# Kernel tuning notes

Measured on AMD Instinct MI355X. Metric: run time of the kernel, lower is better.

## Reference

```python
import jax, jax.numpy as jnp
import numpy as np

A, D, F = 2048, 64, 12  # atoms, depth, filter_length


def _chemconv(x, conn, bond, filters):
    # x: (A, D); conn: (A, A, F); bond: (A, F, 2); filters: (D, F, D+2)
    # node_connection = conn.transpose(1,2) @ x -> (A, F, D)
    ncon = jnp.einsum('anf,nd->afd', conn, x)
    combined = jnp.concatenate([ncon, bond], axis=2)  # (A, F, D+2)
    # broadcast-multiply by filters then sum over last two dims -> (A, out_depth)
    return jnp.einsum('afc,ofc->ao', combined, filters)


def setup_inputs() -> dict:
    key = jax.random.key(0)
    k1, k2, k3, k4, k5 = jax.random.split(key, 5)
    x = jax.random.normal(k1, (A, D), dtype=jnp.float32)
    conn = jax.random.uniform(k2, (A, A, F), dtype=jnp.float32)
    bond = jax.random.normal(k3, (A, F, 2), dtype=jnp.float32)
    scale = 1.0 / D  # filters.data.normal_() * (1/in_depth)
    f0 = jax.random.normal(k4, (D, F, D + 2), dtype=jnp.float32) * scale
    f1 = jax.random.normal(k5, (D, F, D + 2), dtype=jnp.float32) * scale
    return {
        'node_property_tensor': x,
        'connectivity_tensor': conn,
        'bond_property_tensor': bond,
        'filters0': f0,
        'filters1': f1,
    }


def reference(node_property_tensor, connectivity_tensor, bond_property_tensor, filters0, filters1):
    x = node_property_tensor
    out = x
    for filt in (filters0, filters1):
        # each ChemConv layer is applied twice (same weights), per the torch code
        out = jax.nn.relu(_chemconv(out, connectivity_tensor, bond_property_tensor, filt))
        out = _chemconv(out, connectivity_tensor, bond_property_tensor, filt)
        out = out + x  # residual to the original block input
        out = jax.nn.relu(out)
    return out
```

## Files before the change

kernel.cpp:

```cpp
#include <hip/hip_runtime.h>


#define A_N 2048
#define D_N 64
#define F_N 12
#define K_TOTAL (A_N * F_N)
#define NSPLIT 32
#define KSEG (K_TOTAL / NSPLIT)
#define BK 64
#define NKB (KSEG / BK)

typedef short short8 __attribute__((ext_vector_type(8)));
typedef float f32x16 __attribute__((ext_vector_type(16)));

#define GLOAD16(ldsp, gp)                                                        \
  __builtin_amdgcn_global_load_lds(                                              \
      (const __attribute__((address_space(1))) void*)(gp),                       \
      (__attribute__((address_space(3))) void*)(ldsp), 16, 0, 0)

#define VMWAIT(n) asm volatile("s_waitcnt vmcnt(" #n ")" ::: "memory")

__device__ __forceinline__ unsigned pk_bf16(float a, float b) {
  unsigned ua = __float_as_uint(a);
  unsigned ub = __float_as_uint(b);
  ua += 0x7fffu + ((ua >> 16) & 1u);
  ub += 0x7fffu + ((ub >> 16) & 1u);
  return (ua >> 16) | (ub & 0xffff0000u);
}

__device__ __forceinline__ unsigned short bf16_1(float v) {
  unsigned u = __float_as_uint(v);
  u += 0x7fffu + ((u >> 16) & 1u);
  return (unsigned short)(u >> 16);
}

__global__ void k_prep(const float* __restrict__ x, float* __restrict__ xt,
                       const float* __restrict__ bond, const float* __restrict__ f0,
                       const float* __restrict__ f1, float* __restrict__ bt0,
                       float* __restrict__ bt1) {
  int t = threadIdx.x;
  if (blockIdx.x < 32) {
    __shared__ float ld[64][65];
    int m0 = blockIdx.x * 64;
    int r = t >> 2, cq = (t & 3) * 16;
    const float4* src = (const float4*)(x + (size_t)(m0 + r) * 64 + cq);
#pragma unroll
    for (int i = 0; i < 4; ++i) {
      float4 v = src[i];
      ld[r][cq + i * 4 + 0] = v.x;
      ld[r][cq + i * 4 + 1] = v.y;
      ld[r][cq + i * 4 + 2] = v.z;
      ld[r][cq + i * 4 + 3] = v.w;
    }
    __syncthreads();
    int c = t >> 2, ml0 = (t & 3) * 16;
    float4* dst = (float4*)(xt + (size_t)c * 2048 + m0 + ml0);
#pragma unroll
    for (int i = 0; i < 4; ++i) {
      float4 v;
      v.x = ld[ml0 + i * 4 + 0][c];
      v.y = ld[ml0 + i * 4 + 1][c];
      v.z = ld[ml0 + i * 4 + 2][c];
      v.w = ld[ml0 + i * 4 + 3][c];
      dst[i] = v;
    }
  } else {
    int b = blockIdx.x - 32;
    int a = (b & 31) * 64 + (t & 63);
    int o = (b >> 5) * 4 + (t >> 6);
    float s0 = 0.f, s1 = 0.f;
#pragma unroll
    for (int f = 0; f < F_N; ++f) {
#pragma unroll
      for (int j = 0; j < 2; ++j) {
        float bv = bond[a * 24 + f * 2 + j];
        s0 += bv * f0[o * 792 + f * 66 + 64 + j];
        s1 += bv * f1[o * 792 + f * 66 + 64 + j];
      }
    }
    bt0[o * 2048 + a] = s0;
    bt1[o * 2048 + a] = s1;
  }
}

__global__ void k_cvt(const float* __restrict__ conn, unsigned short* __restrict__ connt) {
  int t = threadIdx.x;
  int kb = blockIdx.x, ks = blockIdx.y, atile = blockIdx.z;
  const float* src = conn + (size_t)(atile * 128) * K_TOTAL + ks * KSEG + kb * 64;
  unsigned short* dst = connt + (size_t)((atile * NSPLIT + ks) * NKB + kb) * 8192;
  int r0 = t >> 3, c0 = (t & 7) * 8;
#pragma unroll
  for (int i = 0; i < 4; ++i) {
    int row = r0 + i * 32;
    const float4* s4 = (const float4*)(src + (size_t)row * K_TOTAL + c0);
    float4 a = s4[0], b = s4[1];
    uint4 p;
    p.x = pk_bf16(a.x, a.y);
    p.y = pk_bf16(a.z, a.w);
    p.z = pk_bf16(b.x, b.y);
    p.w = pk_bf16(b.z, b.w);
    *(uint4*)(dst + row * 64 + c0) = p;
  }
}

__global__ void k_g(const float* __restrict__ vt, const float* __restrict__ filt,
                    unsigned short* __restrict__ gtt, int rep) {
  __shared__ __align__(16) float WT[64][12];
  __shared__ __align__(16) unsigned short sg[6144];
  int o = blockIdx.y, bx = blockIdx.x;
  int t = threadIdx.x;
  for (int i = t; i < 768; i += 256) {
    int d = i / 12, f = i % 12;
    WT[d][f] = filt[o * 792 + f * 66 + d];
  }
  __syncthreads();
  int n0 = bx * 512 + t;
  unsigned short* gbase = gtt + (size_t)(bx * 96) * 4096 + o * 64;
  for (int r = 0; r < rep; ++r) {
    float acc0[12], acc1[12];
#pragma unroll
    for (int f = 0; f < 12; ++f) { acc0[f] = 0.f; acc1[f] = 0.f; }
#pragma unroll 4
    for (int d = 0; d < 64; ++d) {
      float v0 = vt[d * 2048 + n0];
      float v1 = vt[d * 2048 + n0 + 256];
      const float4* wp = (const float4*)WT[d];
      float4 w0 = wp[0], w1 = wp[1], w2 = wp[2];
      acc0[0] += v0 * w0.x;  acc0[1] += v0 * w0.y;  acc0[2]  += v0 * w0.z;  acc0[3]  += v0 * w0.w;
      acc0[4] += v0 * w1.x;  acc0[5] += v0 * w1.y;  acc0[6]  += v0 * w1.z;  acc0[7]  += v0 * w1.w;
      acc0[8] += v0 * w2.x;  acc0[9] += v0 * w2.y;  acc0[10] += v0 * w2.z;  acc0[11] += v0 * w2.w;
      acc1[0] += v1 * w0.x;  acc1[1] += v1 * w0.y;  acc1[2]  += v1 * w0.z;  acc1[3]  += v1 * w0.w;
      acc1[4] += v1 * w1.x;  acc1[5] += v1 * w1.y;  acc1[6]  += v1 * w1.z;  acc1[7]  += v1 * w1.w;
      acc1[8] += v1 * w2.x;  acc1[9] += v1 * w2.y;  acc1[10] += v1 * w2.z;  acc1[11] += v1 * w2.w;
    }
#pragma unroll
    for (int f = 0; f < F_N; ++f) {
      sg[t * 12 + f] = bf16_1(acc0[f]);
      sg[t * 12 + 3072 + f] = bf16_1(acc1[f]);
    }
    __syncthreads();
#pragma unroll
    for (int j = 0; j < 3; ++j) {
      int m = t + j * 256;
      *(uint4*)(gbase + (size_t)(m >> 3) * 4096 + (m & 7) * 8) =
          *(const uint4*)(sg + m * 8);
    }
    __syncthreads();
  }
}

__launch_bounds__(256, 2)
__global__ void k_big(const unsigned short* __restrict__ connt,
                      const unsigned short* __restrict__ gtt, float* __restrict__ part) {
  __shared__ __align__(16) unsigned short smem[36864];
  int t = threadIdx.x, lane = t & 63, w = t >> 6;
  int atile = blockIdx.x, ks = blockIdx.y;
  const unsigned short* ct = connt + (size_t)(atile * NSPLIT + ks) * (NKB * 8192);
  const unsigned short* gs = gtt + (size_t)ks * (NKB * 4096);

  int rl = lane >> 3, sl = lane & 7;
  int cs = sl ^ rl;

  int cSrc[4], gSrc[2], cDst[4], gDst[2];
#pragma unroll
  for (int j = 0; j < 4; ++j) {
    cSrc[j] = (w * 32 + j * 8 + rl) * 64 + cs * 8;
    cDst[j] = (w * 32 + j * 8) * 64;
  }
#pragma unroll
  for (int j = 0; j < 2; ++j) {
    gSrc[j] = (w * 16 + j * 8 + rl) * 64 + cs * 8;
    gDst[j] = 8192 + (w * 16 + j * 8) * 64;
  }

  f32x16 acc0, acc1;
#pragma unroll
  for (int i = 0; i < 16; ++i) { acc0[i] = 0.f; acc1[i] = 0.f; }

  int oh = w >> 1, ah = w & 1;
  int orow = oh * 32 + (lane & 31);
  int arow = ah * 64 + (lane & 31);
  int sw = lane & 7;
  int khalf = lane >> 5;

#pragma unroll
  for (int p = 0; p < 2; ++p) {
    unsigned short* base = smem + p * 12288;
#pragma unroll
    for (int j = 0; j < 4; ++j) GLOAD16(base + cDst[j], ct + p * 8192 + cSrc[j]);
#pragma unroll
    for (int j = 0; j < 2; ++j) GLOAD16(base + gDst[j], gs + p * 4096 + gSrc[j]);
  }

#pragma unroll
  for (int kb = 0; kb < NKB; ++kb) {
    if (kb < NKB - 1) VMWAIT(6);
    else VMWAIT(0);
    __builtin_amdgcn_s_barrier();
    asm volatile("" ::: "memory");
    if (kb + 2 < NKB) {
      unsigned short* base = smem + ((kb + 2) % 3) * 12288;
#pragma unroll
      for (int j = 0; j < 4; ++j) GLOAD16(base + cDst[j], ct + (kb + 2) * 8192 + cSrc[j]);
#pragma unroll
      for (int j = 0; j < 2; ++j) GLOAD16(base + gDst[j], gs + (kb + 2) * 4096 + gSrc[j]);
    }
    const unsigned short* cb = smem + (kb % 3) * 12288;
    const unsigned short* gb = cb + 8192;
#pragma unroll
    for (int kk = 0; kk < 4; ++kk) {
      int c = kk * 2 + khalf;
      int coff = ((c ^ sw) << 3);
      short8 af = *(const short8*)(gb + orow * 64 + coff);
      short8 b0 = *(const short8*)(cb + arow * 64 + coff);
      short8 b1 = *(const short8*)(cb + (arow + 32) * 64 + coff);
      acc0 = __builtin_amdgcn_mfma_f32_32x32x16_bf16(af, b0, acc0, 0, 0, 0);
      acc1 = __builtin_amdgcn_mfma_f32_32x32x16_bf16(af, b1, acc1, 0, 0, 0);
    }
  }

  float* pp = part + (size_t)ks * (64 * 2048);
  int a0 = atile * 128 + ah * 64 + (lane & 31);
  int ob = oh * 32 + 4 * khalf;
#pragma unroll
  for (int rg = 0; rg < 16; ++rg) {
    int o = ob + (rg & 3) + 8 * (rg >> 2);
    pp[o * 2048 + a0] = acc0[rg];
    pp[o * 2048 + a0 + 32] = acc1[rg];
  }
}

__global__ void k_reduce(const float* __restrict__ part, const float* __restrict__ bt,
                         const float* __restrict__ xt, float* __restrict__ curt,
                         float* __restrict__ outp, int residual, int final_layer, int rep) {
  __shared__ float4 buf[128];
  int t = threadIdx.x;
  int i4 = blockIdx.x * 128 + (t & 127);
  int half = t >> 7;
  int sbase = half * 16;
  for (int r = 0; r < rep; ++r) {
    float4 s = {0.f, 0.f, 0.f, 0.f};
#pragma unroll
    for (int k = 0; k < 16; ++k) {
      float4 p = ((const float4*)part)[(size_t)(sbase + k) * 32768 + i4];
      s.x += p.x; s.y += p.y; s.z += p.z; s.w += p.w;
    }
    if (half) buf[t & 127] = s;
    __syncthreads();
    if (!half) {
      float4 q = buf[t];
      float4 b = ((const float4*)bt)[i4];
      s.x += q.x + b.x; s.y += q.y + b.y; s.z += q.z + b.z; s.w += q.w + b.w;
      if (residual) {
        float4 rr = ((const float4*)xt)[i4];
        s.x += rr.x; s.y += rr.y; s.z += rr.z; s.w += rr.w;
      }
      s.x = fmaxf(s.x, 0.f); s.y = fmaxf(s.y, 0.f);
      s.z = fmaxf(s.z, 0.f); s.w = fmaxf(s.w, 0.f);
      ((float4*)curt)[i4] = s;
      if (final_layer) {
        int idx = i4 * 4;
        int o = idx >> 11, m = idx & 2047;
        outp[(m + 0) * 64 + o] = s.x;
        outp[(m + 1) * 64 + o] = s.y;
        outp[(m + 2) * 64 + o] = s.z;
        outp[(m + 3) * 64 + o] = s.w;
      }
    }
    __syncthreads();
  }
}

extern "C" void kernel_launch(void* const* d_in, const int* in_sizes, int n_in,
                              void* d_out, int out_size, void* d_ws, size_t ws_size,
                              hipStream_t stream) {
  const float* x    = (const float*)d_in[0];
  const float* conn = (const float*)d_in[1];
  const float* bond = (const float*)d_in[2];
  const float* f0   = (const float*)d_in[3];
  const float* f1   = (const float*)d_in[4];
  float* out = (float*)d_out;

  char* ws = (char*)d_ws;
  float* xt   = (float*)(ws + 0);
  float* curt = (float*)(ws + 524288);
  float* bt0  = (float*)(ws + 1048576);
  float* bt1  = (float*)(ws + 1572864);
  unsigned short* gtt = (unsigned short*)(ws + 2097152);
  float* part = (float*)(ws + 5242880);
  unsigned short* connt = (unsigned short*)(ws + 33554432);

  k_prep<<<544, 256, 0, stream>>>(x, xt, bond, f0, f1, bt0, bt1);
  k_cvt<<<dim3(NKB, NSPLIT, 16), 256, 0, stream>>>(conn, connt);

  for (int layer = 0; layer < 4; ++layer) {
    const float* filt = (layer < 2) ? f0 : f1;
    const float* bt   = (layer < 2) ? bt0 : bt1;
    const float* vin  = (layer == 0) ? xt : curt;
    k_g<<<dim3(4, 64), 256, 0, stream>>>(vin, filt, gtt, (layer == 3) ? 17 : 1);
    k_big<<<dim3(16, NSPLIT), 256, 0, stream>>>(connt, gtt, part);
    k_reduce<<<256, 256, 0, stream>>>(part, bt, xt, curt, out, layer & 1, layer == 3,
                                      (layer == 3) ? 17 : 1);
  }
}
```

Baseline: 551.8 us.

## Halve k_big tile, merge prep and convert kernels, drop repeat loops

k_big now covers 64 atoms per block instead of 128, giving 1024 blocks with a smaller LDS footprint and launch bounds of 3 blocks per CU. The goal is more parallelism and occupancy, at the cost of reloading each G tile twice as often. The separate prep and bf16-convert kernels are merged into one launch to save a kernel launch. The previous code repeated k_g and k_reduce 17 times in the last layer, apparently as padding, and that artificial repeat is removed.

```diff
diff --git a/kernel.cpp b/kernel.cpp
--- a/kernel.cpp
+++ b/kernel.cpp
@@ -34,14 +34,15 @@
   return (unsigned short)(u >> 16);
 }
 
-__global__ void k_prep(const float* __restrict__ x, float* __restrict__ xt,
-                       const float* __restrict__ bond, const float* __restrict__ f0,
-                       const float* __restrict__ f1, float* __restrict__ bt0,
-                       float* __restrict__ bt1) {
-  int t = threadIdx.x;
-  if (blockIdx.x < 32) {
+__global__ void k_pre(const float* __restrict__ x, float* __restrict__ xt,
+                      const float* __restrict__ bond, const float* __restrict__ f0,
+                      const float* __restrict__ f1, float* __restrict__ bt0,
+                      float* __restrict__ bt1, const float* __restrict__ conn,
+                      unsigned short* __restrict__ connt) {
+  int t = threadIdx.x, b = blockIdx.x;
+  if (b < 32) {
     __shared__ float ld[64][65];
-    int m0 = blockIdx.x * 64;
+    int m0 = b * 64;
     int r = t >> 2, cq = (t & 3) * 16;
     const float4* src = (const float4*)(x + (size_t)(m0 + r) * 64 + cq);
 #pragma unroll
@@ -64,10 +65,10 @@
       v.w = ld[ml0 + i * 4 + 3][c];
       dst[i] = v;
     }
-  } else {
-    int b = blockIdx.x - 32;
-    int a = (b & 31) * 64 + (t & 63);
-    int o = (b >> 5) * 4 + (t >> 6);
+  } else if (b < 544) {
+    int b2 = b - 32;
+    int a = (b2 & 31) * 64 + (t & 63);
+    int o = (b2 >> 5) * 4 + (t >> 6);
     float s0 = 0.f, s1 = 0.f;
 #pragma unroll
     for (int f = 0; f < F_N; ++f) {
@@ -80,31 +81,31 @@
     }
     bt0[o * 2048 + a] = s0;
     bt1[o * 2048 + a] = s1;
-  }
-}
-
-__global__ void k_cvt(const float* __restrict__ conn, unsigned short* __restrict__ connt) {
-  int t = threadIdx.x;
-  int kb = blockIdx.x, ks = blockIdx.y, atile = blockIdx.z;
-  const float* src = conn + (size_t)(atile * 128) * K_TOTAL + ks * KSEG + kb * 64;
-  unsigned short* dst = connt + (size_t)((atile * NSPLIT + ks) * NKB + kb) * 8192;
-  int r0 = t >> 3, c0 = (t & 7) * 8;
-#pragma unroll
-  for (int i = 0; i < 4; ++i) {
-    int row = r0 + i * 32;
-    const float4* s4 = (const float4*)(src + (size_t)row * K_TOTAL + c0);
-    float4 a = s4[0], b = s4[1];
-    uint4 p;
-    p.x = pk_bf16(a.x, a.y);
-    p.y = pk_bf16(a.z, a.w);
-    p.z = pk_bf16(b.x, b.y);
-    p.w = pk_bf16(b.z, b.w);
-    *(uint4*)(dst + row * 64 + c0) = p;
+  } else {
+    int i = b - 544;
+    int atile = i / 384;
+    int r2 = i % 384;
+    int ks = r2 / 12, kb = r2 % 12;
+    const float* src = conn + (size_t)(atile * 128) * K_TOTAL + ks * KSEG + kb * 64;
+    unsigned short* dst = connt + (size_t)((atile * NSPLIT + ks) * NKB + kb) * 8192;
+    int r0 = t >> 3, c0 = (t & 7) * 8;
+#pragma unroll
+    for (int q = 0; q < 4; ++q) {
+      int row = r0 + q * 32;
+      const float4* s4 = (const float4*)(src + (size_t)row * K_TOTAL + c0);
+      float4 a = s4[0], bb = s4[1];
+      uint4 p;
+      p.x = pk_bf16(a.x, a.y);
+      p.y = pk_bf16(a.z, a.w);
+      p.z = pk_bf16(bb.x, bb.y);
+      p.w = pk_bf16(bb.z, bb.w);
+      *(uint4*)(dst + row * 64 + c0) = p;
+    }
   }
 }
 
 __global__ void k_g(const float* __restrict__ vt, const float* __restrict__ filt,
-                    unsigned short* __restrict__ gtt, int rep) {
+                    unsigned short* __restrict__ gtt) {
   __shared__ __align__(16) float WT[64][12];
   __shared__ __align__(16) unsigned short sg[6144];
   int o = blockIdx.y, bx = blockIdx.x;
@@ -115,159 +116,149 @@
   }
   __syncthreads();
   int n0 = bx * 512 + t;
+  float acc0[12], acc1[12];
+#pragma unroll
+  for (int f = 0; f < 12; ++f) { acc0[f] = 0.f; acc1[f] = 0.f; }
+#pragma unroll 4
+  for (int d = 0; d < 64; ++d) {
+    float v0 = vt[d * 2048 + n0];
+    float v1 = vt[d * 2048 + n0 + 256];
+    const float4* wp = (const float4*)WT[d];
+    float4 w0 = wp[0], w1 = wp[1], w2 = wp[2];
+    acc0[0] += v0 * w0.x;  acc0[1] += v0 * w0.y;  acc0[2]  += v0 * w0.z;  acc0[3]  += v0 * w0.w;
+    acc0[4] += v0 * w1.x;  acc0[5] += v0 * w1.y;  acc0[6]  += v0 * w1.z;  acc0[7]  += v0 * w1.w;
+    acc0[8] += v0 * w2.x;  acc0[9] += v0 * w2.y;  acc0[10] += v0 * w2.z;  acc0[11] += v0 * w2.w;
+    acc1[0] += v1 * w0.x;  acc1[1] += v1 * w0.y;  acc1[2]  += v1 * w0.z;  acc1[3]  += v1 * w0.w;
+    acc1[4] += v1 * w1.x;  acc1[5] += v1 * w1.y;  acc1[6]  += v1 * w1.z;  acc1[7]  += v1 * w1.w;
+    acc1[8] += v1 * w2.x;  acc1[9] += v1 * w2.y;  acc1[10] += v1 * w2.z;  acc1[11] += v1 * w2.w;
+  }
+#pragma unroll
+  for (int f = 0; f < F_N; ++f) {
+    sg[t * 12 + f] = bf16_1(acc0[f]);
+    sg[t * 12 + 3072 + f] = bf16_1(acc1[f]);
+  }
+  __syncthreads();
   unsigned short* gbase = gtt + (size_t)(bx * 96) * 4096 + o * 64;
-  for (int r = 0; r < rep; ++r) {
-    float acc0[12], acc1[12];
-#pragma unroll
-    for (int f = 0; f < 12; ++f) { acc0[f] = 0.f; acc1[f] = 0.f; }
-#pragma unroll 4
-    for (int d = 0; d < 64; ++d) {
-      float v0 = vt[d * 2048 + n0];
-      float v1 = vt[d * 2048 + n0 + 256];
-      const float4* wp = (const float4*)WT[d];
-      float4 w0 = wp[0], w1 = wp[1], w2 = wp[2];
-      acc0[0] += v0 * w0.x;  acc0[1] += v0 * w0.y;  acc0[2]  += v0 * w0.z;  acc0[3]  += v0 * w0.w;
-      acc0[4] += v0 * w1.x;  acc0[5] += v0 * w1.y;  acc0[6]  += v0 * w1.z;  acc0[7]  += v0 * w1.w;
-      acc0[8] += v0 * w2.x;  acc0[9] += v0 * w2.y;  acc0[10] += v0 * w2.z;  acc0[11] += v0 * w2.w;
-      acc1[0] += v1 * w0.x;  acc1[1] += v1 * w0.y;  acc1[2]  += v1 * w0.z;  acc1[3]  += v1 * w0.w;
-      acc1[4] += v1 * w1.x;  acc1[5] += v1 * w1.y;  acc1[6]  += v1 * w1.z;  acc1[7]  += v1 * w1.w;
-      acc1[8] += v1 * w2.x;  acc1[9] += v1 * w2.y;  acc1[10] += v1 * w2.z;  acc1[11] += v1 * w2.w;
-    }
-#pragma unroll
-    for (int f = 0; f < F_N; ++f) {
-      sg[t * 12 + f] = bf16_1(acc0[f]);
-      sg[t * 12 + 3072 + f] = bf16_1(acc1[f]);
-    }
-    __syncthreads();
-#pragma unroll
-    for (int j = 0; j < 3; ++j) {
-      int m = t + j * 256;
-      *(uint4*)(gbase + (size_t)(m >> 3) * 4096 + (m & 7) * 8) =
-          *(const uint4*)(sg + m * 8);
-    }
-    __syncthreads();
-  }
-}
-
-__launch_bounds__(256, 2)
+#pragma unroll
+  for (int j = 0; j < 3; ++j) {
+    int m = t + j * 256;
+    *(uint4*)(gbase + (size_t)(m >> 3) * 4096 + (m & 7) * 8) = *(const uint4*)(sg + m * 8);
+  }
+}
+
+__launch_bounds__(256, 3)
 __global__ void k_big(const unsigned short* __restrict__ connt,
                       const unsigned short* __restrict__ gtt, float* __restrict__ part) {
-  __shared__ __align__(16) unsigned short smem[36864];
+  __shared__ __align__(16) unsigned short smem[24576];
   int t = threadIdx.x, lane = t & 63, w = t >> 6;
   int atile = blockIdx.x, ks = blockIdx.y;
-  const unsigned short* ct = connt + (size_t)(atile * NSPLIT + ks) * (NKB * 8192);
+  int a128 = atile >> 1, half = atile & 1;
+  const unsigned short* ct =
+      connt + (size_t)(a128 * NSPLIT + ks) * (NKB * 8192) + half * 4096;
   const unsigned short* gs = gtt + (size_t)ks * (NKB * 4096);
 
   int rl = lane >> 3, sl = lane & 7;
   int cs = sl ^ rl;
 
-  int cSrc[4], gSrc[2], cDst[4], gDst[2];
-#pragma unroll
-  for (int j = 0; j < 4; ++j) {
-    cSrc[j] = (w * 32 + j * 8 + rl) * 64 + cs * 8;
-    cDst[j] = (w * 32 + j * 8) * 64;
-  }
+  int cSrc[2], gSrc[2], cDst[2], gDst[2];
 #pragma unroll
   for (int j = 0; j < 2; ++j) {
-    gSrc[j] = (w * 16 + j * 8 + rl) * 64 + cs * 8;
-    gDst[j] = 8192 + (w * 16 + j * 8) * 64;
-  }
-
-  f32x16 acc0, acc1;
-#pragma unroll
-  for (int i = 0; i < 16; ++i) { acc0[i] = 0.f; acc1[i] = 0.f; }
+    int row = w * 16 + j * 8 + rl;
+    cSrc[j] = row * 64 + cs * 8;
+    cDst[j] = (w * 16 + j * 8) * 64;
+    gSrc[j] = row * 64 + cs * 8;
+    gDst[j] = 4096 + (w * 16 + j * 8) * 64;
+  }
+
+  f32x16 acc0;
+#pragma unroll
+  for (int i = 0; i < 16; ++i) acc0[i] = 0.f;
 
   int oh = w >> 1, ah = w & 1;
   int orow = oh * 32 + (lane & 31);
-  int arow = ah * 64 + (lane & 31);
+  int arow = ah * 32 + (lane & 31);
   int sw = lane & 7;
   int khalf = lane >> 5;
 
 #pragma unroll
   for (int p = 0; p < 2; ++p) {
-    unsigned short* base = smem + p * 12288;
-#pragma unroll
-    for (int j = 0; j < 4; ++j) GLOAD16(base + cDst[j], ct + p * 8192 + cSrc[j]);
+    unsigned short* base = smem + p * 8192;
+#pragma unroll
+    for (int j = 0; j < 2; ++j) GLOAD16(base + cDst[j], ct + p * 8192 + cSrc[j]);
 #pragma unroll
     for (int j = 0; j < 2; ++j) GLOAD16(base + gDst[j], gs + p * 4096 + gSrc[j]);
   }
 
 #pragma unroll
   for (int kb = 0; kb < NKB; ++kb) {
-    if (kb < NKB - 1) VMWAIT(6);
+    if (kb < NKB - 1) VMWAIT(4);
     else VMWAIT(0);
     __builtin_amdgcn_s_barrier();
     asm volatile("" ::: "memory");
     if (kb + 2 < NKB) {
-      unsigned short* base = smem + ((kb + 2) % 3) * 12288;
-#pragma unroll
-      for (int j = 0; j < 4; ++j) GLOAD16(base + cDst[j], ct + (kb + 2) * 8192 + cSrc[j]);
+      unsigned short* base = smem + ((kb + 2) % 3) * 8192;
+#pragma unroll
+      for (int j = 0; j < 2; ++j) GLOAD16(base + cDst[j], ct + (kb + 2) * 8192 + cSrc[j]);
 #pragma unroll
       for (int j = 0; j < 2; ++j) GLOAD16(base + gDst[j], gs + (kb + 2) * 4096 + gSrc[j]);
     }
-    const unsigned short* cb = smem + (kb % 3) * 12288;
-    const unsigned short* gb = cb + 8192;
+    const unsigned short* cb = smem + (kb % 3) * 8192;
+    const unsigned short* gb = cb + 4096;
 #pragma unroll
     for (int kk = 0; kk < 4; ++kk) {
       int c = kk * 2 + khalf;
       int coff = ((c ^ sw) << 3);
       short8 af = *(const short8*)(gb + orow * 64 + coff);
       short8 b0 = *(const short8*)(cb + arow * 64 + coff);
-      short8 b1 = *(const short8*)(cb + (arow + 32) * 64 + coff);
       acc0 = __builtin_amdgcn_mfma_f32_32x32x16_bf16(af, b0, acc0, 0, 0, 0);
-      acc1 = __builtin_amdgcn_mfma_f32_32x32x16_bf16(af, b1, acc1, 0, 0, 0);
     }
   }
 
   float* pp = part + (size_t)ks * (64 * 2048);
-  int a0 = atile * 128 + ah * 64 + (lane & 31);
+  int a0 = atile * 64 + ah * 32 + (lane & 31);
   int ob = oh * 32 + 4 * khalf;
 #pragma unroll
   for (int rg = 0; rg < 16; ++rg) {
     int o = ob + (rg & 3) + 8 * (rg >> 2);
     pp[o * 2048 + a0] = acc0[rg];
-    pp[o * 2048 + a0 + 32] = acc1[rg];
-  }
-}
-
-__global__ void k_reduce(const float* __restrict__ part, const float* __restrict__ bt,
-                         const float* __restrict__ xt, float* __restrict__ curt,
-                         float* __restrict__ outp, int residual, int final_layer, int rep) {
+  }
+}
+
+__global__ void k_red(const float* __restrict__ part, const float* __restrict__ bt,
+                      const float* __restrict__ xt, float* __restrict__ curt,
+                      float* __restrict__ outp, int residual, int final_layer) {
   __shared__ float4 buf[128];
   int t = threadIdx.x;
   int i4 = blockIdx.x * 128 + (t & 127);
   int half = t >> 7;
   int sbase = half * 16;
-  for (int r = 0; r < rep; ++r) {
-    float4 s = {0.f, 0.f, 0.f, 0.f};
-#pragma unroll
-    for (int k = 0; k < 16; ++k) {
-      float4 p = ((const float4*)part)[(size_t)(sbase + k) * 32768 + i4];
-      s.x += p.x; s.y += p.y; s.z += p.z; s.w += p.w;
-    }
-    if (half) buf[t & 127] = s;
-    __syncthreads();
-    if (!half) {
-      float4 q = buf[t];
-      float4 b = ((const float4*)bt)[i4];
-      s.x += q.x + b.x; s.y += q.y + b.y; s.z += q.z + b.z; s.w += q.w + b.w;
-      if (residual) {
-        float4 rr = ((const float4*)xt)[i4];
-        s.x += rr.x; s.y += rr.y; s.z += rr.z; s.w += rr.w;
-      }
-      s.x = fmaxf(s.x, 0.f); s.y = fmaxf(s.y, 0.f);
-      s.z = fmaxf(s.z, 0.f); s.w = fmaxf(s.w, 0.f);
-      ((float4*)curt)[i4] = s;
-      if (final_layer) {
-        int idx = i4 * 4;
-        int o = idx >> 11, m = idx & 2047;
-        outp[(m + 0) * 64 + o] = s.x;
-        outp[(m + 1) * 64 + o] = s.y;
-        outp[(m + 2) * 64 + o] = s.z;
-        outp[(m + 3) * 64 + o] = s.w;
-      }
-    }
-    __syncthreads();
+  float4 s = {0.f, 0.f, 0.f, 0.f};
+#pragma unroll
+  for (int k = 0; k < 16; ++k) {
+    float4 p = ((const float4*)part)[(size_t)(sbase + k) * 32768 + i4];
+    s.x += p.x; s.y += p.y; s.z += p.z; s.w += p.w;
+  }
+  if (half) buf[t & 127] = s;
+  __syncthreads();
+  if (!half) {
+    float4 q = buf[t];
+    float4 b = ((const float4*)bt)[i4];
+    s.x += q.x + b.x; s.y += q.y + b.y; s.z += q.z + b.z; s.w += q.w + b.w;
+    if (residual) {
+      float4 rr = ((const float4*)xt)[i4];
+      s.x += rr.x; s.y += rr.y; s.z += rr.z; s.w += rr.w;
+    }
+    s.x = fmaxf(s.x, 0.f); s.y = fmaxf(s.y, 0.f);
+    s.z = fmaxf(s.z, 0.f); s.w = fmaxf(s.w, 0.f);
+    ((float4*)curt)[i4] = s;
+    if (final_layer) {
+      int idx = i4 * 4;
+      int o = idx >> 11, m = idx & 2047;
+      outp[(m + 0) * 64 + o] = s.x;
+      outp[(m + 1) * 64 + o] = s.y;
+      outp[(m + 2) * 64 + o] = s.z;
+      outp[(m + 3) * 64 + o] = s.w;
+    }
   }
 }
 
@@ -290,16 +281,14 @@
   float* part = (float*)(ws + 5242880);
   unsigned short* connt = (unsigned short*)(ws + 33554432);
 
-  k_prep<<<544, 256, 0, stream>>>(x, xt, bond, f0, f1, bt0, bt1);
-  k_cvt<<<dim3(NKB, NSPLIT, 16), 256, 0, stream>>>(conn, connt);
+  k_pre<<<6688, 256, 0, stream>>>(x, xt, bond, f0, f1, bt0, bt1, conn, connt);
 
   for (int layer = 0; layer < 4; ++layer) {
     const float* filt = (layer < 2) ? f0 : f1;
     const float* bt   = (layer < 2) ? bt0 : bt1;
     const float* vin  = (layer == 0) ? xt : curt;
-    k_g<<<dim3(4, 64), 256, 0, stream>>>(vin, filt, gtt, (layer == 3) ? 17 : 1);
-    k_big<<<dim3(16, NSPLIT), 256, 0, stream>>>(connt, gtt, part);
-    k_reduce<<<256, 256, 0, stream>>>(part, bt, xt, curt, out, layer & 1, layer == 3,
-                                      (layer == 3) ? 17 : 1);
-  }
-}
+    k_g<<<dim3(4, 64), 256, 0, stream>>>(vin, filt, gtt);
+    k_big<<<dim3(32, NSPLIT), 256, 0, stream>>>(connt, gtt, part);
+    k_red<<<256, 256, 0, stream>>>(part, bt, xt, curt, out, layer & 1, layer == 3);
+  }
+}
```

After: 450.3 us. 1.23x faster.
